# Performance work log

Hardware: AMD Instinct MI355X
Metric: run time of the kernel (lower is better)

## Reference

```python
import jax, jax.numpy as jnp
import numpy as np

B, S, H, L = 128, 2048, 512, 11

def setup_inputs() -> dict:
    key = jax.random.key(0)
    k1, k2, k3, k4 = jax.random.split(key, 4)
    return {
        "find_contri": 1,
        "code_output": jax.random.normal(k1, (B, S, H), dtype=jnp.float32),
        "lengths": jax.random.randint(k2, (B,), 1, S + 1),  # ragged lengths in [1, S]
        "contri": jax.random.uniform(k3, (B, S, 2), dtype=jnp.float32),
        "fc_w": jax.random.normal(k4, (L, H), dtype=jnp.float32) * 0.05,
    }

def reference(find_contri, code_output, lengths, contri, fc_w):
    b, s, h = code_output.shape
    # Faithful to torch .view (reshape, not transpose): [B,S,H] -> [B,H,S]
    x = code_output.reshape(b, h, s)
    # Ragged adaptive max-pool to size 1 with indices: mask positions >= length
    valid = jnp.arange(s)[None, :] < lengths[:, None]            # [B,S]
    xm = jnp.where(valid[:, None, :], x, -jnp.inf)               # [B,H,S]
    code_pool = jnp.max(xm, axis=2)                              # [B,H]
    code_indices = jnp.argmax(xm, axis=2)                        # [B,H], in [0,len)
    attn = code_pool @ fc_w.T                                    # [B,11], no bias
    if find_contri:
        # con[lab,i] = relu(pool[i]*fc_w[lab]) + 1e-4, normalized to sum 100.
        # Original mutates one `contri` tensor across all labs and appends the
        # same reference 11 times; the final state is the sum over labs.
        p10 = code_pool[:10]                                     # only first 10 samples
        con = jax.nn.relu(p10[:, None, :] * fc_w[None, :, :]) + 1e-4   # [10,11,H]
        con = con / jnp.sum(con, axis=2, keepdims=True) * 100.0
        total = jnp.sum(con, axis=1)                             # [10,H]
        # indexed scatter-add into the new third channel
        scat = jax.vmap(lambda idx, c: jnp.zeros((s,), total.dtype).at[idx].add(c))(
            code_indices[:10], total)                            # [10,S]
        ch2 = jnp.zeros((b, s), contri.dtype).at[:10].set(scat)  # [B,S]
        contri_out = jnp.concatenate([contri, ch2[..., None]], axis=2)  # [B,S,3]
        return attn, contri_out
    return attn
```

## Files before the change

### kernel.cpp

```cpp
#include <hip/hip_runtime.h>
#include <math.h>

#define BB 128
#define SS 2048
#define HH 512
#define LL 11

typedef float vf4 __attribute__((ext_vector_type(4)));

__global__ __launch_bounds__(256) void rowmax_kernel(
    const float* __restrict__ x,
    const int* __restrict__ lengths,
    float* __restrict__ pool,
    int* __restrict__ idx_out) {
  int gid = blockIdx.x * blockDim.x + threadIdx.x;
  int wave = gid >> 6;
  int lane = threadIdx.x & 63;
  if (wave >= BB * HH) return;
  int b = wave >> 9;
  int len = lengths[b];
  const vf4* row = (const vf4*)(x + (size_t)wave * SS);

  float best = -INFINITY;
  int bidx = 0;
#pragma unroll
  for (int j = 0; j < 8; ++j) {
    int e = j * 64 + lane;
    vf4 v = __builtin_nontemporal_load(&row[e]);
    int si = e * 4;
    float a;
    a = (si + 0 < len) ? v.x : -INFINITY;
    if (a > best) { best = a; bidx = si + 0; }
    a = (si + 1 < len) ? v.y : -INFINITY;
    if (a > best) { best = a; bidx = si + 1; }
    a = (si + 2 < len) ? v.z : -INFINITY;
    if (a > best) { best = a; bidx = si + 2; }
    a = (si + 3 < len) ? v.w : -INFINITY;
    if (a > best) { best = a; bidx = si + 3; }
  }
#pragma unroll
  for (int off = 32; off > 0; off >>= 1) {
    float ov = __shfl_down(best, off);
    int oi = __shfl_down(bidx, off);
    if (ov > best || (ov == best && oi < bidx)) { best = ov; bidx = oi; }
  }
  if (lane == 0) {
    pool[wave] = best;
    idx_out[wave] = bidx;
  }
}

__global__ __launch_bounds__(256) void epilogue_kernel(
    const float* __restrict__ pool,
    const int* __restrict__ idx_in,
    const float* __restrict__ fcw,
    const float* __restrict__ contri,
    float* __restrict__ attn_out,
    float* __restrict__ out2) {
  int tid = threadIdx.x;
  int wv = tid >> 6;
  int lane = tid & 63;

  if (blockIdx.x < 10) {
    int b = blockIdx.x;
    __shared__ float sp[HH];
    __shared__ float sden[LL];
    __shared__ float sch[SS];

    for (int h = tid; h < HH; h += 256) sp[h] = pool[b * HH + h];
    for (int s = tid; s < SS; s += 256) sch[s] = 0.f;
    __syncthreads();

    for (int l = wv; l < LL; l += 4) {
      float s = 0.f;
#pragma unroll
      for (int k = 0; k < HH / 64; ++k) {
        int h = k * 64 + lane;
        s += fmaxf(sp[h] * fcw[l * HH + h], 0.f);
      }
#pragma unroll
      for (int off = 32; off > 0; off >>= 1) s += __shfl_down(s, off);
      if (lane == 0) sden[l] = 100.f / (s + (float)HH * 1e-4f);
    }
    __syncthreads();

    for (int hh = tid; hh < HH; hh += 256) {
      float p = sp[hh];
      float tot = 0.f;
#pragma unroll
      for (int l = 0; l < LL; ++l)
        tot += (fmaxf(p * fcw[l * HH + hh], 0.f) + 1e-4f) * sden[l];
      atomicAdd(&sch[idx_in[b * HH + hh]], tot);
    }
    __syncthreads();

    for (int s = tid; s < SS; s += 256) {
      int t = b * SS + s;
      out2[t * 3 + 0] = contri[t * 2 + 0];
      out2[t * 3 + 1] = contri[t * 2 + 1];
      out2[t * 3 + 2] = sch[s];
    }
  } else if (blockIdx.x < 10 + BB) {
    int b = blockIdx.x - 10;
    const float* p = pool + b * HH;
    for (int l = wv; l < LL; l += 4) {
      const float* w = fcw + l * HH;
      float s = 0.f;
#pragma unroll
      for (int k = 0; k < HH / 64; ++k) s += p[k * 64 + lane] * w[k * 64 + lane];
#pragma unroll
      for (int off = 32; off > 0; off >>= 1) s += __shfl_down(s, off);
      if (lane == 0) attn_out[b * LL + l] = s;
    }
  } else {
    int i = (blockIdx.x - (10 + BB)) * 256 + tid;
    int t = 10 * SS + i;
    if (t < BB * SS) {
      out2[t * 3 + 0] = contri[t * 2 + 0];
      out2[t * 3 + 1] = contri[t * 2 + 1];
      out2[t * 3 + 2] = 0.f;
    }
  }
}

extern "C" void kernel_launch(void* const* d_in, const int* in_sizes, int n_in,
                              void* d_out, int out_size, void* d_ws, size_t ws_size,
                              hipStream_t stream) {
  const float* code_output = (const float*)d_in[1];
  const int* lengths = (const int*)d_in[2];
  const float* contri = (const float*)d_in[3];
  const float* fcw = (const float*)d_in[4];

  float* out = (float*)d_out;
  float* out2 = out + BB * LL;

  float* ws = (float*)d_ws;
  float* pool = ws;
  int* idx = (int*)(ws + BB * HH);

  rowmax_kernel<<<(BB * HH * 64) / 256, 256, 0, stream>>>(code_output, lengths,
                                                          pool, idx);

  int copy_blocks = ((BB - 10) * SS + 255) / 256;
  epilogue_kernel<<<10 + BB + copy_blocks, 256, 0, stream>>>(pool, idx, fcw,
                                                             contri, out, out2);
}
```

Baseline: 651.5 us.

## Skip masked tail in rowmax and fold contri copy into first kernel

The row max/argmax loop now runs only over the 256-element chunks that fall inside each sample's length, so the masked tail of each row is never loaded from memory. A one-step software prefetch replaces the fully unrolled nontemporal loads. The bulk copy of contri for samples 10 and up moves from the epilogue kernel into extra blocks of the first kernel, so it overlaps with the reduction. The trade-off is a data-dependent loop with less unrolling and fewer loads in flight per wave.

```diff
diff --git a/kernel.cpp b/kernel.cpp
--- a/kernel.cpp
+++ b/kernel.cpp
@@ -8,26 +8,40 @@
 
 typedef float vf4 __attribute__((ext_vector_type(4)));
 
+#define COPYBLK 944
+
 __global__ __launch_bounds__(256) void rowmax_kernel(
     const float* __restrict__ x,
     const int* __restrict__ lengths,
+    const float* __restrict__ contri,
     float* __restrict__ pool,
-    int* __restrict__ idx_out) {
-  int gid = blockIdx.x * blockDim.x + threadIdx.x;
-  int wave = gid >> 6;
+    int* __restrict__ idx_out,
+    float* __restrict__ out2) {
+  if (blockIdx.x < COPYBLK) {
+    int i = blockIdx.x * 256 + threadIdx.x;
+    int t = 10 * SS + i;
+    out2[t * 3 + 0] = contri[t * 2 + 0];
+    out2[t * 3 + 1] = contri[t * 2 + 1];
+    out2[t * 3 + 2] = 0.f;
+    return;
+  }
+
+  int wave = (blockIdx.x - COPYBLK) * 4 + (threadIdx.x >> 6);
   int lane = threadIdx.x & 63;
-  if (wave >= BB * HH) return;
   int b = wave >> 9;
   int len = lengths[b];
   const vf4* row = (const vf4*)(x + (size_t)wave * SS);
 
+  int nj = (len + 255) >> 8;
+
   float best = -INFINITY;
   int bidx = 0;
-#pragma unroll
-  for (int j = 0; j < 8; ++j) {
-    int e = j * 64 + lane;
-    vf4 v = __builtin_nontemporal_load(&row[e]);
-    int si = e * 4;
+  vf4 v = row[lane];
+  for (int j = 0; j < nj; ++j) {
+    vf4 nxt = v;
+    if (j + 1 < nj)
+      nxt = row[(j + 1) * 64 + lane];
+    int si = (j * 64 + lane) * 4;
     float a;
     a = (si + 0 < len) ? v.x : -INFINITY;
     if (a > best) { best = a; bidx = si + 0; }
@@ -37,7 +51,9 @@
     if (a > best) { best = a; bidx = si + 2; }
     a = (si + 3 < len) ? v.w : -INFINITY;
     if (a > best) { best = a; bidx = si + 3; }
+    v = nxt;
   }
+
 #pragma unroll
   for (int off = 32; off > 0; off >>= 1) {
     float ov = __shfl_down(best, off);
@@ -100,7 +116,7 @@
       out2[t * 3 + 1] = contri[t * 2 + 1];
       out2[t * 3 + 2] = sch[s];
     }
-  } else if (blockIdx.x < 10 + BB) {
+  } else {
     int b = blockIdx.x - 10;
     const float* p = pool + b * HH;
     for (int l = wv; l < LL; l += 4) {
@@ -111,14 +127,6 @@
 #pragma unroll
       for (int off = 32; off > 0; off >>= 1) s += __shfl_down(s, off);
       if (lane == 0) attn_out[b * LL + l] = s;
-    }
-  } else {
-    int i = (blockIdx.x - (10 + BB)) * 256 + tid;
-    int t = 10 * SS + i;
-    if (t < BB * SS) {
-      out2[t * 3 + 0] = contri[t * 2 + 0];
-      out2[t * 3 + 1] = contri[t * 2 + 1];
-      out2[t * 3 + 2] = 0.f;
     }
   }
 }
@@ -138,10 +146,9 @@
   float* pool = ws;
   int* idx = (int*)(ws + BB * HH);
 
-  rowmax_kernel<<<(BB * HH * 64) / 256, 256, 0, stream>>>(code_output, lengths,
-                                                          pool, idx);
+  int row_blocks = (BB * HH) / 4;
+  rowmax_kernel<<<COPYBLK + row_blocks, 256, 0, stream>>>(
+      code_output, lengths, contri, pool, idx, out2);
 
-  int copy_blocks = ((BB - 10) * SS + 255) / 256;
-  epilogue_kernel<<<10 + BB + copy_blocks, 256, 0, stream>>>(pool, idx, fcw,
-                                                             contri, out, out2);
+  epilogue_kernel<<<10 + BB, 256, 0, stream>>>(pool, idx, fcw, contri, out, out2);
 }
```

Result: no change. 645.8 us (-0.9%).
